# Optimization experiments

Hardware: AMD Instinct MI355X
Metric: run time of the kernel (lower is better)

The kernel has to match this reference:

```python
import jax, jax.numpy as jnp
import numpy as np

T, H, E, I, K = 4096, 1024, 8, 1024, 2  # tokens, hidden, experts, intermediate, top_k


def setup_inputs() -> dict:
    key = jax.random.key(0)
    k1, k2, k3, k4, k5 = jax.random.split(key, 5)
    x = jax.random.normal(k1, (T, H), dtype=jnp.float32)
    router_logits = jax.random.normal(k2, (T, E), dtype=jnp.float32)
    per_expert_scale = jnp.ones((E,), dtype=jnp.float32)
    # FusedMoE layout: w13 = fused [gate; up] projection [E, 2I, H], w2 = down [E, H, I]
    w13 = jax.random.normal(k3, (E, 2 * I, H), dtype=jnp.float32) * 0.02
    w2 = jax.random.normal(k4, (E, H, I), dtype=jnp.float32) * 0.02
    return {"x": x, "router_logits": router_logits,
            "per_expert_scale": per_expert_scale, "w13": w13, "w2": w2}


def reference(x, router_logits, per_expert_scale, w13, w2):
    # --- Gemma4 routing: softmax over ALL experts -> top-k -> renormalize ---
    _, topk_ids = jax.lax.top_k(router_logits, K)              # [T, K] int32
    probs = jax.nn.softmax(router_logits, axis=-1)             # [T, E]
    indicator = jax.nn.one_hot(topk_ids, E, dtype=probs.dtype).sum(axis=-2)  # [T, E]
    gate = indicator * probs
    renorm = gate.sum(axis=-1, keepdims=True)
    renorm = jnp.where(renorm > 0.0, renorm, 1.0)
    dispatch = gate / renorm                                   # zero off top-k
    # per_expert_scale folded into routing weights (only top-k slots nonzero)
    combine_w = dispatch * per_expert_scale[None, :]           # [T, E]

    # --- expert FFN (gelu gate * up -> down), combined with routing weights ---
    w1, w3 = w13[:, :I, :], w13[:, I:, :]                      # [E, I, H] each
    g = jnp.einsum('th,eih->tei', x, w1)                       # gate proj
    u = jnp.einsum('th,eih->tei', x, w3)                       # up proj
    h = jax.nn.gelu(g, approximate=False) * u                  # exact GELU (torch default)
    y = jnp.einsum('tei,ehi->teh', h, w2)                      # down proj
    out = jnp.einsum('te,teh->th', combine_w, y)               # weighted combine
    return out
```

## Files before the change

kernel.cpp:

```cpp
#include <hip/hip_runtime.h>
#include <hip/hip_bf16.h>

#define T_TOK 4096
#define H_DIM 1024
#define E_NUM 8
#define I_DIM 1024
#define PAD_CAP 9216

typedef __attribute__((ext_vector_type(4))) float f32x4;
typedef __attribute__((ext_vector_type(8))) short bf16x8;

__device__ __forceinline__ unsigned short f2b(float f) {
  union { float f; unsigned int u; } v; v.f = f;
  unsigned int r = v.u + 0x7fffu + ((v.u >> 16) & 1u);
  return (unsigned short)(r >> 16);
}

__device__ __forceinline__ void async_copy16(const void* g, void* l) {
  __builtin_amdgcn_global_load_lds(
      (const __attribute__((address_space(1))) void*)g,
      (__attribute__((address_space(3))) void*)l, 16, 0, 0);
}

__global__ __launch_bounds__(1024) void k_route(
    const float* __restrict__ logits, const float* __restrict__ scale,
    int* __restrict__ pad_off, int* __restrict__ perm,
    int* __restrict__ inv, float* __restrict__ cw) {
  __shared__ int s_cnt[E_NUM], s_off[E_NUM], s_cur[E_NUM];
  const int tid = threadIdx.x;
  if (tid < E_NUM) s_cnt[tid] = 0;
  __syncthreads();
  int e0[4], e1[4];
#pragma unroll
  for (int it = 0; it < 4; ++it) {
    int t = it * 1024 + tid;
    float l[E_NUM];
    *(float4*)(l)     = *(const float4*)(logits + (size_t)t * E_NUM);
    *(float4*)(l + 4) = *(const float4*)(logits + (size_t)t * E_NUM + 4);
    float m = l[0];
#pragma unroll
    for (int i = 1; i < E_NUM; ++i) m = fmaxf(m, l[i]);
    float p[E_NUM]; float s = 0.f;
#pragma unroll
    for (int i = 0; i < E_NUM; ++i) { p[i] = expf(l[i] - m); s += p[i]; }
    int i0 = 0; float b0 = l[0];
#pragma unroll
    for (int i = 1; i < E_NUM; ++i) if (l[i] > b0) { b0 = l[i]; i0 = i; }
    int i1 = -1; float b1 = -1e30f;
#pragma unroll
    for (int i = 0; i < E_NUM; ++i) if (i != i0 && l[i] > b1) { b1 = l[i]; i1 = i; }
    float g0 = p[i0] / s, g1 = p[i1] / s;
    float r = g0 + g1;
    cw[t * 2]     = g0 / r * scale[i0];
    cw[t * 2 + 1] = g1 / r * scale[i1];
    e0[it] = i0; e1[it] = i1;
    atomicAdd(&s_cnt[i0], 1);
    atomicAdd(&s_cnt[i1], 1);
  }
  __syncthreads();
  if (tid == 0) {
    int off = 0;
    for (int e = 0; e < E_NUM; ++e) {
      s_off[e] = off; s_cur[e] = off; pad_off[e] = off;
      off += (s_cnt[e] + 127) & ~127;
    }
    pad_off[E_NUM] = off;
  }
  __syncthreads();
#pragma unroll
  for (int it = 0; it < 4; ++it) {
    int t = it * 1024 + tid;
    int sl0 = atomicAdd(&s_cur[e0[it]], 1);
    perm[sl0] = t * 2;     inv[t * 2] = sl0;
    int sl1 = atomicAdd(&s_cur[e1[it]], 1);
    perm[sl1] = t * 2 + 1; inv[t * 2 + 1] = sl1;
  }
  __syncthreads();
  for (int e = 0; e < E_NUM; ++e) {
    int start = s_off[e] + s_cnt[e];
    int end   = s_off[e] + ((s_cnt[e] + 127) & ~127);
    for (int i = start + tid; i < end; i += 1024) perm[i] = -1;
  }
}

__global__ void k_conv3(const float* __restrict__ x, const float* __restrict__ w13,
                        const float* __restrict__ w2,
                        unsigned short* __restrict__ xb,
                        unsigned short* __restrict__ w13b,
                        unsigned short* __restrict__ w2b) {
  int b = blockIdx.x;
  const float* src; unsigned short* dst; size_t base;
  if (b < 2048)       { src = x;   dst = xb;   base = (size_t)b * 2048; }
  else if (b < 10240) { src = w13; dst = w13b; base = (size_t)(b - 2048) * 2048; }
  else                { src = w2;  dst = w2b;  base = (size_t)(b - 10240) * 2048; }
  size_t i = base + (size_t)threadIdx.x * 8;
  float4 f0 = *(const float4*)(src + i);
  float4 f1 = *(const float4*)(src + i + 4);
  uint4 pk;
  pk.x = (unsigned)f2b(f0.x) | ((unsigned)f2b(f0.y) << 16);
  pk.y = (unsigned)f2b(f0.z) | ((unsigned)f2b(f0.w) << 16);
  pk.z = (unsigned)f2b(f1.x) | ((unsigned)f2b(f1.y) << 16);
  pk.w = (unsigned)f2b(f1.z) | ((unsigned)f2b(f1.w) << 16);
  *(uint4*)(dst + i) = pk;
}

__global__ __launch_bounds__(256, 2) void k_gemm1(
    const unsigned short* __restrict__ xbf,
    const unsigned short* __restrict__ w13b,
    const int* __restrict__ perm, const int* __restrict__ pad_off,
    unsigned short* __restrict__ h_buf) {
  __shared__ __align__(16) unsigned short a_lds[128 * 64];
  __shared__ __align__(16) unsigned short b_lds[128 * 64];
  const int tid = threadIdx.x;
  const int wave = tid >> 6, lane = tid & 63;
  const int row0 = blockIdx.y * 128;
  if (row0 >= pad_off[E_NUM]) return;
  int e = 0;
#pragma unroll
  for (int i = 1; i < E_NUM; ++i) if (row0 >= pad_off[i]) e = i;
  const int iBase = blockIdx.x * 64;

  const int srcChunk = (lane & 7) ^ ((lane >> 3) & 7);

  const unsigned short* agbase[4];
#pragma unroll
  for (int j = 0; j < 4; ++j) {
    int r = j * 32 + wave * 8 + (lane >> 3);
    int p = perm[row0 + r];
    int tok = (p < 0) ? 0 : (p >> 1);
    agbase[j] = xbf + (size_t)tok * H_DIM + srcChunk * 8;
  }
  const unsigned short* bgbase[4];
#pragma unroll
  for (int j = 0; j < 4; ++j) {
    int brow = j * 32 + wave * 8 + (lane >> 3);
    int seg = brow >> 5, half = seg & 1;
    int col = iBase + (seg >> 1) * 32 + (brow & 31);
    bgbase[j] = w13b + ((size_t)e * 2 * I_DIM + half * I_DIM + col) * H_DIM + srcChunk * 8;
  }

  f32x4 acc[4][4];
#pragma unroll
  for (int mi = 0; mi < 4; ++mi)
#pragma unroll
    for (int ni = 0; ni < 4; ++ni) acc[mi][ni] = (f32x4)(0.f);

  const int wm = wave >> 1, wn = wave & 1;
  const int ml = lane & 15, quad = lane >> 4;

  for (int k0 = 0; k0 < H_DIM; k0 += 64) {
    __syncthreads();
#pragma unroll
    for (int j = 0; j < 4; ++j)
      async_copy16(agbase[j] + k0, a_lds + (j * 256 + wave * 64) * 8);
#pragma unroll
    for (int j = 0; j < 4; ++j)
      async_copy16(bgbase[j] + k0, b_lds + (j * 256 + wave * 64) * 8);
    __syncthreads();
#pragma unroll
    for (int ks = 0; ks < 2; ++ks) {
      const int ch = ((ks * 4 + quad) ^ (ml & 7)) * 8;
      bf16x8 af[4], bfr[4];
#pragma unroll
      for (int mi = 0; mi < 4; ++mi)
        af[mi] = *(const bf16x8*)(a_lds + (wm * 64 + mi * 16 + ml) * 64 + ch);
#pragma unroll
      for (int ni = 0; ni < 4; ++ni)
        bfr[ni] = *(const bf16x8*)(b_lds + (wn * 64 + ni * 16 + ml) * 64 + ch);
#pragma unroll
      for (int mi = 0; mi < 4; ++mi)
#pragma unroll
        for (int ni = 0; ni < 4; ++ni)
          acc[mi][ni] = __builtin_amdgcn_mfma_f32_16x16x32_bf16(af[mi], bfr[ni], acc[mi][ni], 0, 0, 0);
    }
  }
#pragma unroll
  for (int mi = 0; mi < 4; ++mi) {
#pragma unroll
    for (int nc = 0; nc < 2; ++nc) {
      f32x4 g = acc[mi][nc];
      f32x4 uu = acc[mi][nc + 2];
#pragma unroll
      for (int r = 0; r < 4; ++r) {
        int row = row0 + wm * 64 + mi * 16 + quad * 4 + r;
        int col = iBase + wn * 32 + nc * 16 + ml;
        float gg = g[r];
        float hv = 0.5f * gg * (1.f + erff(gg * 0.7071067811865475f)) * uu[r];
        h_buf[(size_t)row * I_DIM + col] = f2b(hv);
      }
    }
  }
}

__global__ __launch_bounds__(256, 2) void k_gemm2(
    const unsigned short* __restrict__ h_buf,
    const unsigned short* __restrict__ w2b,
    const int* __restrict__ pad_off,
    unsigned short* __restrict__ y) {
  __shared__ __align__(16) unsigned short a_lds[128 * 64];
  __shared__ __align__(16) unsigned short b_lds[64 * 64];
  const int tid = threadIdx.x;
  const int wave = tid >> 6, lane = tid & 63;
  const int row0 = blockIdx.y * 128;
  if (row0 >= pad_off[E_NUM]) return;
  int e = 0;
#pragma unroll
  for (int i = 1; i < E_NUM; ++i) if (row0 >= pad_off[i]) e = i;
  const int cBase = blockIdx.x * 64;
  const int srcChunk = (lane & 7) ^ ((lane >> 3) & 7);

  const unsigned short* agbase[4];
#pragma unroll
  for (int j = 0; j < 4; ++j) {
    int r = j * 32 + wave * 8 + (lane >> 3);
    agbase[j] = h_buf + (size_t)(row0 + r) * I_DIM + srcChunk * 8;
  }
  const unsigned short* bgbase[2];
#pragma unroll
  for (int j = 0; j < 2; ++j) {
    int brow = j * 32 + wave * 8 + (lane >> 3);
    bgbase[j] = w2b + ((size_t)e * H_DIM + cBase + brow) * I_DIM + srcChunk * 8;
  }
  f32x4 acc[2][4];
#pragma unroll
  for (int mi = 0; mi < 2; ++mi)
#pragma unroll
    for (int ni = 0; ni < 4; ++ni) acc[mi][ni] = (f32x4)(0.f);
  const int ml = lane & 15, quad = lane >> 4;

  for (int k0 = 0; k0 < I_DIM; k0 += 64) {
    __syncthreads();
#pragma unroll
    for (int j = 0; j < 4; ++j)
      async_copy16(agbase[j] + k0, a_lds + (j * 256 + wave * 64) * 8);
#pragma unroll
    for (int j = 0; j < 2; ++j)
      async_copy16(bgbase[j] + k0, b_lds + (j * 256 + wave * 64) * 8);
    __syncthreads();
#pragma unroll
    for (int ks = 0; ks < 2; ++ks) {
      const int ch = ((ks * 4 + quad) ^ (ml & 7)) * 8;
      bf16x8 af[2], bfr[4];
#pragma unroll
      for (int mi = 0; mi < 2; ++mi)
        af[mi] = *(const bf16x8*)(a_lds + (wave * 32 + mi * 16 + ml) * 64 + ch);
#pragma unroll
      for (int ni = 0; ni < 4; ++ni)
        bfr[ni] = *(const bf16x8*)(b_lds + (ni * 16 + ml) * 64 + ch);
#pragma unroll
      for (int mi = 0; mi < 2; ++mi)
#pragma unroll
        for (int ni = 0; ni < 4; ++ni)
          acc[mi][ni] = __builtin_amdgcn_mfma_f32_16x16x32_bf16(af[mi], bfr[ni], acc[mi][ni], 0, 0, 0);
    }
  }
#pragma unroll
  for (int mi = 0; mi < 2; ++mi) {
#pragma unroll
    for (int ni = 0; ni < 4; ++ni) {
#pragma unroll
      for (int r = 0; r < 4; ++r) {
        int row = row0 + wave * 32 + mi * 16 + quad * 4 + r;
        int col = cBase + ni * 16 + ml;
        y[(size_t)row * H_DIM + col] = f2b(acc[mi][ni][r]);
      }
    }
  }
}

__global__ void k_combine(const unsigned short* __restrict__ y,
                          const int* __restrict__ inv, const float* __restrict__ cw,
                          float* __restrict__ out) {
  const int t = blockIdx.x;
  const int c = threadIdx.x * 4;
  int s0 = inv[t * 2], s1 = inv[t * 2 + 1];
  float c0 = cw[t * 2], c1 = cw[t * 2 + 1];
  uint2 a = *(const uint2*)(y + (size_t)s0 * H_DIM + c);
  uint2 b = *(const uint2*)(y + (size_t)s1 * H_DIM + c);
  union { unsigned v; float f; } w;
  float4 o;
  float alo, ahi, blo, bhi;
  w.v = a.x << 16;          alo = w.f;
  w.v = a.x & 0xffff0000u;  ahi = w.f;
  w.v = b.x << 16;          blo = w.f;
  w.v = b.x & 0xffff0000u;  bhi = w.f;
  o.x = c0 * alo + c1 * blo;
  o.y = c0 * ahi + c1 * bhi;
  w.v = a.y << 16;          alo = w.f;
  w.v = a.y & 0xffff0000u;  ahi = w.f;
  w.v = b.y << 16;          blo = w.f;
  w.v = b.y & 0xffff0000u;  bhi = w.f;
  o.z = c0 * alo + c1 * blo;
  o.w = c0 * ahi + c1 * bhi;
  *(float4*)(out + (size_t)t * H_DIM + c) = o;
}

extern "C" void kernel_launch(void* const* d_in, const int* in_sizes, int n_in,
                              void* d_out, int out_size, void* d_ws, size_t ws_size,
                              hipStream_t stream) {
  const float* x      = (const float*)d_in[0];
  const float* logits = (const float*)d_in[1];
  const float* scale  = (const float*)d_in[2];
  const float* w13    = (const float*)d_in[3];
  const float* w2     = (const float*)d_in[4];
  float* out = (float*)d_out;

  char* ws = (char*)d_ws;
  int*   pad_off = (int*)(ws + 128);
  float* cw      = (float*)(ws + 65536);
  int*   perm    = (int*)(ws + 131072);
  int*   inv     = (int*)(ws + 196608);
  unsigned short* xb    = (unsigned short*)(ws + 0x40000);
  unsigned short* h_buf = (unsigned short*)(ws + 0x900000);
  unsigned short* w13b  = (unsigned short*)(ws + 0x1C00000);
  unsigned short* ybuf  = w13b;
  unsigned short* w2b   = (unsigned short*)(ws + 0x3C00000);

  k_route<<<1, 1024, 0, stream>>>(logits, scale, pad_off, perm, inv, cw);
  k_conv3<<<14336, 256, 0, stream>>>(x, w13, w2, xb, w13b, w2b);
  k_gemm1<<<dim3(16, PAD_CAP / 128), 256, 0, stream>>>(xb, w13b, perm, pad_off, h_buf);
  k_gemm2<<<dim3(16, PAD_CAP / 128), 256, 0, stream>>>(h_buf, w2b, pad_off, ybuf);
  k_combine<<<T_TOK, 256, 0, stream>>>(ybuf, inv, cw, out);
}
```

Baseline: 246.3 us.

## Parallelize routing across blocks and fuse it into the conversion kernel

Replaces the single-block routing kernel with sixteen routing blocks that run inside the bf16 conversion launch. Each block writes per-block expert counts, a small scan kernel then computes padded offsets, and a scatter kernel fills perm and inv. This is meant to remove the serial single-workgroup routing stage. In exchange it adds two extra small kernel launches.

```diff
diff --git a/kernel.cpp b/kernel.cpp
--- a/kernel.cpp
+++ b/kernel.cpp
@@ -6,6 +6,7 @@
 #define E_NUM 8
 #define I_DIM 1024
 #define PAD_CAP 9216
+#define RBLK 16
 
 typedef __attribute__((ext_vector_type(4))) float f32x4;
 typedef __attribute__((ext_vector_type(8))) short bf16x8;
@@ -22,18 +23,20 @@
       (__attribute__((address_space(3))) void*)l, 16, 0, 0);
 }
 
-__global__ __launch_bounds__(1024) void k_route(
-    const float* __restrict__ logits, const float* __restrict__ scale,
-    int* __restrict__ pad_off, int* __restrict__ perm,
-    int* __restrict__ inv, float* __restrict__ cw) {
-  __shared__ int s_cnt[E_NUM], s_off[E_NUM], s_cur[E_NUM];
-  const int tid = threadIdx.x;
-  if (tid < E_NUM) s_cnt[tid] = 0;
-  __syncthreads();
-  int e0[4], e1[4];
-#pragma unroll
-  for (int it = 0; it < 4; ++it) {
-    int t = it * 1024 + tid;
+__global__ __launch_bounds__(256) void k_prep(
+    const float* __restrict__ x, const float* __restrict__ logits,
+    const float* __restrict__ scale,
+    const float* __restrict__ w13, const float* __restrict__ w2,
+    unsigned short* __restrict__ xb, unsigned short* __restrict__ w13b,
+    unsigned short* __restrict__ w2b,
+    int* __restrict__ tids, float* __restrict__ cw, int* __restrict__ cnt) {
+  const int b = blockIdx.x;
+  if (b < RBLK) {
+    __shared__ int s_cnt[E_NUM];
+    const int tid = threadIdx.x;
+    if (tid < E_NUM) s_cnt[tid] = 0;
+    __syncthreads();
+    int t = b * 256 + tid;
     float l[E_NUM];
     *(float4*)(l)     = *(const float4*)(logits + (size_t)t * E_NUM);
     *(float4*)(l + 4) = *(const float4*)(logits + (size_t)t * E_NUM + 4);
@@ -53,46 +56,18 @@
     float r = g0 + g1;
     cw[t * 2]     = g0 / r * scale[i0];
     cw[t * 2 + 1] = g1 / r * scale[i1];
-    e0[it] = i0; e1[it] = i1;
+    tids[t * 2] = i0; tids[t * 2 + 1] = i1;
     atomicAdd(&s_cnt[i0], 1);
     atomicAdd(&s_cnt[i1], 1);
-  }
-  __syncthreads();
-  if (tid == 0) {
-    int off = 0;
-    for (int e = 0; e < E_NUM; ++e) {
-      s_off[e] = off; s_cur[e] = off; pad_off[e] = off;
-      off += (s_cnt[e] + 127) & ~127;
-    }
-    pad_off[E_NUM] = off;
-  }
-  __syncthreads();
-#pragma unroll
-  for (int it = 0; it < 4; ++it) {
-    int t = it * 1024 + tid;
-    int sl0 = atomicAdd(&s_cur[e0[it]], 1);
-    perm[sl0] = t * 2;     inv[t * 2] = sl0;
-    int sl1 = atomicAdd(&s_cur[e1[it]], 1);
-    perm[sl1] = t * 2 + 1; inv[t * 2 + 1] = sl1;
-  }
-  __syncthreads();
-  for (int e = 0; e < E_NUM; ++e) {
-    int start = s_off[e] + s_cnt[e];
-    int end   = s_off[e] + ((s_cnt[e] + 127) & ~127);
-    for (int i = start + tid; i < end; i += 1024) perm[i] = -1;
-  }
-}
-
-__global__ void k_conv3(const float* __restrict__ x, const float* __restrict__ w13,
-                        const float* __restrict__ w2,
-                        unsigned short* __restrict__ xb,
-                        unsigned short* __restrict__ w13b,
-                        unsigned short* __restrict__ w2b) {
-  int b = blockIdx.x;
+    __syncthreads();
+    if (tid < E_NUM) cnt[b * E_NUM + tid] = s_cnt[tid];
+    return;
+  }
+  const int cb = b - RBLK;
   const float* src; unsigned short* dst; size_t base;
-  if (b < 2048)       { src = x;   dst = xb;   base = (size_t)b * 2048; }
-  else if (b < 10240) { src = w13; dst = w13b; base = (size_t)(b - 2048) * 2048; }
-  else                { src = w2;  dst = w2b;  base = (size_t)(b - 10240) * 2048; }
+  if (cb < 2048)       { src = x;   dst = xb;   base = (size_t)cb * 2048; }
+  else if (cb < 10240) { src = w13; dst = w13b; base = (size_t)(cb - 2048) * 2048; }
+  else                 { src = w2;  dst = w2b;  base = (size_t)(cb - 10240) * 2048; }
   size_t i = base + (size_t)threadIdx.x * 8;
   float4 f0 = *(const float4*)(src + i);
   float4 f1 = *(const float4*)(src + i + 4);
@@ -102,6 +77,49 @@
   pk.z = (unsigned)f2b(f1.x) | ((unsigned)f2b(f1.y) << 16);
   pk.w = (unsigned)f2b(f1.z) | ((unsigned)f2b(f1.w) << 16);
   *(uint4*)(dst + i) = pk;
+}
+
+__global__ __launch_bounds__(256) void k_scan(
+    const int* __restrict__ cnt, int* __restrict__ pad_off,
+    int* __restrict__ base, int* __restrict__ perm) {
+  __shared__ int s_tot[E_NUM], s_off[E_NUM + 1];
+  const int tid = threadIdx.x;
+  if (tid == 0) {
+    int off = 0;
+    for (int e = 0; e < E_NUM; ++e) {
+      int tot = 0;
+      for (int b = 0; b < RBLK; ++b) tot += cnt[b * E_NUM + e];
+      s_tot[e] = tot;
+      s_off[e] = off; pad_off[e] = off;
+      int run = off;
+      for (int b = 0; b < RBLK; ++b) { base[b * E_NUM + e] = run; run += cnt[b * E_NUM + e]; }
+      off += (tot + 127) & ~127;
+    }
+    s_off[E_NUM] = off; pad_off[E_NUM] = off;
+  }
+  __syncthreads();
+  for (int e = 0; e < E_NUM; ++e) {
+    int start = s_off[e] + s_tot[e];
+    int end   = s_off[e + 1];
+    for (int i = start + tid; i < end; i += 256) perm[i] = -1;
+  }
+}
+
+__global__ __launch_bounds__(256) void k_scatter(
+    const int* __restrict__ tids, const int* __restrict__ base,
+    int* __restrict__ perm, int* __restrict__ inv) {
+  __shared__ int l_cnt[E_NUM];
+  const int b = blockIdx.x, tid = threadIdx.x;
+  if (tid < E_NUM) l_cnt[tid] = 0;
+  __syncthreads();
+  int t = b * 256 + tid;
+  int i0 = tids[t * 2], i1 = tids[t * 2 + 1];
+  int r0 = atomicAdd(&l_cnt[i0], 1);
+  int s0 = base[b * E_NUM + i0] + r0;
+  perm[s0] = t * 2; inv[t * 2] = s0;
+  int r1 = atomicAdd(&l_cnt[i1], 1);
+  int s1 = base[b * E_NUM + i1] + r1;
+  perm[s1] = t * 2 + 1; inv[t * 2 + 1] = s1;
 }
 
 __global__ __launch_bounds__(256, 2) void k_gemm1(
@@ -307,6 +325,9 @@
 
   char* ws = (char*)d_ws;
   int*   pad_off = (int*)(ws + 128);
+  int*   cnt     = (int*)(ws + 1024);
+  int*   base    = (int*)(ws + 2048);
+  int*   tids    = (int*)(ws + 4096);
   float* cw      = (float*)(ws + 65536);
   int*   perm    = (int*)(ws + 131072);
   int*   inv     = (int*)(ws + 196608);
@@ -316,8 +337,10 @@
   unsigned short* ybuf  = w13b;
   unsigned short* w2b   = (unsigned short*)(ws + 0x3C00000);
 
-  k_route<<<1, 1024, 0, stream>>>(logits, scale, pad_off, perm, inv, cw);
-  k_conv3<<<14336, 256, 0, stream>>>(x, w13, w2, xb, w13b, w2b);
+  k_prep<<<14336 + RBLK, 256, 0, stream>>>(x, logits, scale, w13, w2,
+                                           xb, w13b, w2b, tids, cw, cnt);
+  k_scan<<<1, 256, 0, stream>>>(cnt, pad_off, base, perm);
+  k_scatter<<<RBLK, 256, 0, stream>>>(tids, base, perm, inv);
   k_gemm1<<<dim3(16, PAD_CAP / 128), 256, 0, stream>>>(xb, w13b, perm, pad_off, h_buf);
   k_gemm2<<<dim3(16, PAD_CAP / 128), 256, 0, stream>>>(h_buf, w2b, pad_off, ybuf);
   k_combine<<<T_TOK, 256, 0, stream>>>(ybuf, inv, cw, out);
```

New measurement: 241.8 us. About the same (-1.8%).
